# Performance work log

Hardware: AMD Instinct MI355X
Metric: run time of the kernel (lower is better)

## Reference

```python
import jax, jax.numpy as jnp
import numpy as np

B, M, S, P, A, D, H = 16, 8, 100, 40, 3, 128, 8
HD = D // H  # head dim = 16
EPS = 1e-5


def _layernorm(x, g, b):
    mu = jnp.mean(x, axis=-1, keepdims=True)
    var = jnp.mean(jnp.square(x - mu), axis=-1, keepdims=True)
    return (x - mu) * jax.lax.rsqrt(var + EPS) * g + b


def setup_inputs() -> dict:
    key = jax.random.key(0)
    ks = jax.random.split(key, 20)
    attrs = jax.random.normal(ks[0], (B, M, S, P, A), dtype=jnp.float32)
    valid = (jax.random.uniform(ks[1], (B, M, S, P)) < 0.85).astype(jnp.float32)
    roads = jnp.concatenate([attrs, valid[..., None]], axis=-1)  # (B,M,S,P,A+1)
    agents_emb = jax.random.normal(ks[2], (4, B, M, D), dtype=jnp.float32)

    def xavier(k, shape):
        fan_in, fan_out = shape[-2], shape[-1]
        std = float(np.sqrt(2.0 / (fan_in + fan_out)))
        return jax.random.normal(k, shape, dtype=jnp.float32) * std

    return {
        "roads": roads,
        "agents_emb": agents_emb,
        "map_seeds": xavier(ks[3], (1, 1, D)),
        "lin_w": xavier(ks[4], (A, D)), "lin_b": jnp.zeros((D,)),
        "wq": xavier(ks[5], (D, D)), "wk": xavier(ks[6], (D, D)), "wv": xavier(ks[7], (D, D)),
        "bq": jnp.zeros((D,)), "bk": jnp.zeros((D,)), "bv": jnp.zeros((D,)),
        "out_w": xavier(ks[8], (D, D)), "out_b": jnp.zeros((D,)),
        "ln1_g": jnp.ones((D,)), "ln1_b": jnp.zeros((D,)),
        "w1": xavier(ks[9], (D, 3 * D)), "b1": jnp.zeros((3 * D,)),
        "w2": xavier(ks[10], (3 * D, D)), "b2": jnp.zeros((D,)),
        "ln2_g": jnp.ones((D,)), "ln2_b": jnp.zeros((D,)),
    }


def reference(roads, agents_emb, map_seeds, lin_w, lin_b, wq, wk, wv, bq, bk, bv,
              out_w, out_b, ln1_g, ln1_b, w1, b1, w2, b2, ln2_g, ln2_b):
    N = B * M * S
    last = roads[..., -1]  # (B,M,S,P), exact 0/1 existence flags
    # --- masks (True = padded / ignore) ---
    seg_mask = jnp.sum(last, axis=3) == 0  # (B,M,S)
    pts_mask = (1.0 - last).astype(bool).reshape(N, P)
    all_pts = jnp.all(pts_mask, axis=-1)
    pts_mask = pts_mask.at[:, 0].set(pts_mask[:, 0] & ~all_pts)  # unmask pt 0 of empty segs
    all_seg = jnp.all(seg_mask, axis=-1)
    seg_mask = seg_mask.at[:, :, 0].set(seg_mask[:, :, 0] & ~all_seg)

    # --- point feature projection ---
    feats = roads[..., :A].reshape(N, P, A) @ lin_w + lin_b  # (N,P,D)

    # --- single-query multi-head attention pooling (eval mode: no dropout) ---
    q = (map_seeds.reshape(D) @ wq + bq).reshape(H, HD)  # shared seed query
    k = (feats @ wk + bk).reshape(N, P, H, HD)
    v = (feats @ wv + bv).reshape(N, P, H, HD)
    scores = jnp.einsum('hd,nphd->nhp', q, k) * (HD ** -0.5)  # (N,H,P)
    scores = jnp.where(pts_mask[:, None, :], -1e9, scores)
    attn = jax.nn.softmax(scores, axis=-1)
    ctx = jnp.einsum('nhp,nphd->nhd', attn, v).reshape(N, D)
    emb = _layernorm(ctx @ out_w + out_b, ln1_g, ln1_b)  # (N,D)

    # --- FFN + residual + norm (eval mode: no dropout) ---
    ffn = jax.nn.relu(emb @ w1 + b1) @ w2 + b2
    emb2 = _layernorm(emb + ffn, ln2_g, ln2_b)

    out = emb2.reshape(B, M, S, D).transpose(2, 0, 1, 3)  # (S,B,M,D)
    return out, seg_mask
```

## Files before the change

kernel.cpp:

```cpp
#include <hip/hip_runtime.h>

namespace {
constexpr int Sn = 100;
constexpr int Nn = 12800;
constexpr int OUT0 = 1638400;
}

using bf16x8 = __attribute__((ext_vector_type(8))) short;
using f32x4  = __attribute__((ext_vector_type(4))) float;
#define MFMA16(a, b, c) __builtin_amdgcn_mfma_f32_16x16x32_bf16((a), (b), (c), 0, 0, 0)

__device__ __forceinline__ unsigned short f2bf(float x) {
  unsigned int u = __float_as_uint(x);
  return (unsigned short)((u + 0x7FFFu + ((u >> 16) & 1u)) >> 16);
}
__device__ __forceinline__ float bf2f(unsigned short h) {
  return __uint_as_float(((unsigned int)h) << 16);
}

__global__ __launch_bounds__(128) void k0_precompute(
    const float* __restrict__ ms, const float* __restrict__ wq,
    const float* __restrict__ wk, const float* __restrict__ bq,
    const float* __restrict__ bk, const float* __restrict__ lin_w,
    const float* __restrict__ lin_b, const float* __restrict__ wv,
    const float* __restrict__ bv, const float* __restrict__ out_w,
    float* __restrict__ W4qk, unsigned short* __restrict__ Tf) {
  const int t = threadIdx.x;
  if (blockIdx.x < 8) {
    const int h = blockIdx.x;
    __shared__ float q[128];
    __shared__ float qkh[128];
    __shared__ float qbkh;
    __shared__ float part[128];
    float s = bq[t];
    for (int c = 0; c < 128; ++c) s += ms[c] * wq[c * 128 + t];
    q[t] = s;
    __syncthreads();
    float a = 0.f;
#pragma unroll
    for (int j = 0; j < 16; ++j) a += q[h * 16 + j] * wk[t * 128 + h * 16 + j];
    qkh[t] = a * 0.25f;
    if (t == 0) {
      float b = 0.f;
#pragma unroll
      for (int j = 0; j < 16; ++j) b += q[h * 16 + j] * bk[h * 16 + j];
      qbkh = b * 0.25f;
    }
    __syncthreads();
    const int j = t >> 5, cp = t & 31;
    float p = 0.f;
    for (int c = cp * 4; c < cp * 4 + 4; ++c) {
      const float w4 = (j < 3) ? lin_w[j * 128 + c] : lin_b[c];
      p += w4 * qkh[c];
    }
    part[t] = p;
    __syncthreads();
    if (t < 4) {
      float sum = 0.f;
      for (int i = 0; i < 32; ++i) sum += part[t * 32 + i];
      if (t == 3) sum += qbkh;
      W4qk[t * 8 + h] = sum;
    }
  } else {
    const int hj = blockIdx.x - 8;
    const int h = hj >> 2, j = hj & 3;
    __shared__ float part[128];
    __shared__ float w4wv[16];
    const int cp = t & 7;
    float p = 0.f;
    for (int c = cp * 16; c < cp * 16 + 16; ++c) {
      const float w4 = (j < 3) ? lin_w[j * 128 + c] : lin_b[c];
      p += w4 * wv[c * 128 + (h * 16 + (t >> 3))];
    }
    part[t] = p;
    __syncthreads();
    if (t < 16) {
      float sum = 0.f;
      for (int i = 0; i < 8; ++i) sum += part[t * 8 + i];
      if (j == 3) sum += bv[h * 16 + t];
      w4wv[t] = sum;
    }
    __syncthreads();
    float acc = 0.f;
#pragma unroll
    for (int e2 = 0; e2 < 16; ++e2) acc += w4wv[e2] * out_w[(h * 16 + e2) * 128 + t];
    const int ntT = t >> 4, n16T = t & 15;
    const int quadT = hj >> 3, jT = hj & 7;
    const int slot = ntT * 1024 + (quadT * 16 + n16T) * 8 + jT;
    const unsigned short hh = f2bf(acc);
    Tf[slot] = hh;
    Tf[slot + 512] = f2bf(acc - bf2f(hh));
  }
}

__global__ __launch_bounds__(256) void k0b_repack(
    const float* __restrict__ w1, const float* __restrict__ w2,
    unsigned short* __restrict__ w1f, unsigned short* __restrict__ w2f) {
  const int gid = blockIdx.x * 256 + threadIdx.x;
  const int tile = gid >> 6, lane = gid & 63;
  const int quad = lane >> 4, n16 = lane & 15;
  unsigned short hi[8], lo[8];
  unsigned short* dst;
  if (tile < 96) {
    const int nt = tile >> 2, kk = tile & 3;
    const int n = nt * 16 + n16;
#pragma unroll
    for (int j = 0; j < 8; ++j) {
      const int k = kk * 32 + quad * 8 + j;
      const float v = w1[k * 384 + n];
      hi[j] = f2bf(v); lo[j] = f2bf(v - bf2f(hi[j]));
    }
    dst = w1f + (size_t)tile * 1024 + lane * 8;
  } else {
    const int t2 = tile - 96;
    const int nt2 = t2 / 12, kk2 = t2 % 12;
    const int n = nt2 * 16 + n16;
#pragma unroll
    for (int j = 0; j < 8; ++j) {
      const int k = kk2 * 32 + quad * 8 + j;
      const float v = w2[k * 128 + n];
      hi[j] = f2bf(v); lo[j] = f2bf(v - bf2f(hi[j]));
    }
    dst = w2f + (size_t)(tile - 96) * 1024 + lane * 8;
  }
#pragma unroll
  for (int j = 0; j < 8; ++j) { dst[j] = hi[j]; dst[512 + j] = lo[j]; }
}

__global__ __launch_bounds__(256, 4) void k_all(
    const float* __restrict__ roads, const float* __restrict__ W4qk_g,
    const unsigned short* __restrict__ Tf, const float* __restrict__ out_b,
    const float* __restrict__ ln1_g, const float* __restrict__ ln1_b,
    const unsigned short* __restrict__ w1f, const unsigned short* __restrict__ w2f,
    const float* __restrict__ b1, const float* __restrict__ b2,
    const float* __restrict__ ln2_g, const float* __restrict__ ln2_b,
    float* __restrict__ out) {
  const int t = threadIdx.x;
  const int n0 = blockIdx.x * 16;

  __shared__ union {
    float4 pts[640];
    __align__(16) unsigned short A2[12288];
  } u;
  __shared__ __align__(16) unsigned short A1[4096];
  __shared__ __align__(16) unsigned short ApF[1024];
  __shared__ float w4qk_l[32];
  __shared__ float lnr[16][4][2];

  for (int i = t; i < 640; i += 256)
    u.pts[i] = ((const float4*)roads)[(size_t)n0 * 40 + i];
  if (t < 32) w4qk_l[t] = W4qk_g[t];
  __syncthreads();

  {
    const int sh = t >> 1, seg = sh >> 3, h = sh & 7;
    const int p0 = (t & 1) * 20;
    const float wa = w4qk_l[h], wb = w4qk_l[8 + h];
    const float wc = w4qk_l[16 + h], wd = w4qk_l[24 + h];
    float ax = 0.f, ay = 0.f, az = 0.f, den = 0.f;
    int nv = 0;
    for (int p = p0; p < p0 + 20; ++p) {
      const float4 pt = u.pts[seg * 40 + p];
      if (pt.w != 0.f) {
        const float e = __expf(wd + pt.x * wa + pt.y * wb + pt.z * wc);
        ax += e * pt.x; ay += e * pt.y; az += e * pt.z; den += e; ++nv;
      }
    }
    ax += __shfl_xor(ax, 1); ay += __shfl_xor(ay, 1); az += __shfl_xor(az, 1);
    den += __shfl_xor(den, 1); nv += __shfl_xor(nv, 1);
    if ((t & 1) == 0) {
      if (nv == 0) {
        const float4 z = u.pts[seg * 40];
        ax = z.x; ay = z.y; az = z.z; den = 1.f;
      }
      const float inv = 1.f / den;
      const float v[4] = {ax * inv, ay * inv, az * inv, 1.f};
      ushort4 hi, lo;
      unsigned short* hp = (unsigned short*)&hi;
      unsigned short* lp = (unsigned short*)&lo;
#pragma unroll
      for (int c = 0; c < 4; ++c) { hp[c] = f2bf(v[c]); lp[c] = f2bf(v[c] - bf2f(hp[c])); }
      const int slot = ((h >> 1) * 16 + seg) * 8 + (h & 1) * 4;
      *(ushort4*)&ApF[slot] = hi;
      *(ushort4*)&ApF[512 + slot] = lo;
      if (h == 0) out[OUT0 + n0 + seg] = (nv == 0) ? 1.f : 0.f;
    }
  }
  __syncthreads();

  const int w = t >> 6, lane = t & 63;
  const int quad = lane >> 4, nlane = lane & 15;

  float embv[2][4];
  {
    const bf16x8 ahi = *(const bf16x8*)&ApF[lane * 8];
    const bf16x8 alo = *(const bf16x8*)&ApF[512 + lane * 8];
#pragma unroll
    for (int n2 = 0; n2 < 2; ++n2) {
      const int nt = w * 2 + n2;
      const unsigned short* tp = Tf + (size_t)nt * 1024;
      const bf16x8 bhi = *(const bf16x8*)(tp + lane * 8);
      const bf16x8 blo = *(const bf16x8*)(tp + 512 + lane * 8);
      f32x4 acc = (f32x4){0.f, 0.f, 0.f, 0.f};
      acc = MFMA16(alo, bhi, acc);
      acc = MFMA16(ahi, blo, acc);
      acc = MFMA16(ahi, bhi, acc);
      const float ob = out_b[nt * 16 + nlane];
#pragma unroll
      for (int r = 0; r < 4; ++r) embv[n2][r] = acc[r] + ob;
    }
#pragma unroll
    for (int r = 0; r < 4; ++r) {
      float s = embv[0][r] + embv[1][r];
      float v = embv[0][r] * embv[0][r] + embv[1][r] * embv[1][r];
#pragma unroll
      for (int m = 1; m < 16; m <<= 1) { s += __shfl_xor(s, m); v += __shfl_xor(v, m); }
      if (nlane == 0) { lnr[quad * 4 + r][w][0] = s; lnr[quad * 4 + r][w][1] = v; }
    }
  }
  __syncthreads();
#pragma unroll
  for (int r = 0; r < 4; ++r) {
    const int row = quad * 4 + r;
    const float mu = (lnr[row][0][0] + lnr[row][1][0] + lnr[row][2][0] + lnr[row][3][0]) * (1.f / 128.f);
    const float msq = (lnr[row][0][1] + lnr[row][1][1] + lnr[row][2][1] + lnr[row][3][1]) * (1.f / 128.f);
    const float rstd = rsqrtf(msq - mu * mu + 1e-5f);
#pragma unroll
    for (int n2 = 0; n2 < 2; ++n2) {
      const int col = (w * 2 + n2) * 16 + nlane;
      const float e = (embv[n2][r] - mu) * rstd * ln1_g[col] + ln1_b[col];
      const unsigned short hh = f2bf(e), hl = f2bf(e - bf2f(hh));
      const int kk = col >> 5, q2 = (col >> 3) & 3, j = col & 7;
      const int idx = kk * 512 + (q2 * 16 + row) * 8 + j;
      A1[idx] = hh; A1[2048 + idx] = hl;
    }
  }
  __syncthreads();

#pragma unroll
  for (int nti = 0; nti < 6; ++nti) {
    const int nt = w * 6 + nti;
    f32x4 acc = (f32x4){0.f, 0.f, 0.f, 0.f};
#pragma unroll
    for (int kk = 0; kk < 4; ++kk) {
      const bf16x8 ahi = *(const bf16x8*)&A1[kk * 512 + lane * 8];
      const bf16x8 alo = *(const bf16x8*)&A1[2048 + kk * 512 + lane * 8];
      const unsigned short* wp = w1f + (size_t)(nt * 4 + kk) * 1024;
      const bf16x8 bhi = *(const bf16x8*)(wp + lane * 8);
      const bf16x8 blo = *(const bf16x8*)(wp + 512 + lane * 8);
      acc = MFMA16(alo, bhi, acc);
      acc = MFMA16(ahi, blo, acc);
      acc = MFMA16(ahi, bhi, acc);
    }
    const int col = nt * 16 + nlane;
    const float bias = b1[col];
    const int kk2 = col >> 5, qA = (col >> 3) & 3, jA = col & 7;
#pragma unroll
    for (int r = 0; r < 4; ++r) {
      const float h = fmaxf(acc[r] + bias, 0.f);
      const unsigned short hh = f2bf(h), hl = f2bf(h - bf2f(hh));
      const int idx = kk2 * 512 + (qA * 16 + quad * 4 + r) * 8 + jA;
      u.A2[idx] = hh; u.A2[6144 + idx] = hl;
    }
  }
  __syncthreads();

  f32x4 acc2[2];
  acc2[0] = (f32x4){0.f, 0.f, 0.f, 0.f};
  acc2[1] = (f32x4){0.f, 0.f, 0.f, 0.f};
#pragma unroll 4
  for (int kk2 = 0; kk2 < 12; ++kk2) {
    const bf16x8 ahi = *(const bf16x8*)&u.A2[kk2 * 512 + lane * 8];
    const bf16x8 alo = *(const bf16x8*)&u.A2[6144 + kk2 * 512 + lane * 8];
#pragma unroll
    for (int n2 = 0; n2 < 2; ++n2) {
      const unsigned short* wp = w2f + (size_t)((w * 2 + n2) * 12 + kk2) * 1024;
      const bf16x8 bhi = *(const bf16x8*)(wp + lane * 8);
      const bf16x8 blo = *(const bf16x8*)(wp + 512 + lane * 8);
      acc2[n2] = MFMA16(alo, bhi, acc2[n2]);
      acc2[n2] = MFMA16(ahi, blo, acc2[n2]);
      acc2[n2] = MFMA16(ahi, bhi, acc2[n2]);
    }
  }

  float y[2][4];
#pragma unroll
  for (int n2 = 0; n2 < 2; ++n2) {
    const int col = (w * 2 + n2) * 16 + nlane;
    const float bb = b2[col];
    const int kk = col >> 5, q2 = (col >> 3) & 3, j = col & 7;
#pragma unroll
    for (int r = 0; r < 4; ++r) {
      const int idx = kk * 512 + (q2 * 16 + quad * 4 + r) * 8 + j;
      y[n2][r] = acc2[n2][r] + bb + bf2f(A1[idx]) + bf2f(A1[2048 + idx]);
    }
  }
#pragma unroll
  for (int r = 0; r < 4; ++r) {
    float s = y[0][r] + y[1][r];
    float v = y[0][r] * y[0][r] + y[1][r] * y[1][r];
#pragma unroll
    for (int m = 1; m < 16; m <<= 1) { s += __shfl_xor(s, m); v += __shfl_xor(v, m); }
    if (nlane == 0) { lnr[quad * 4 + r][w][0] = s; lnr[quad * 4 + r][w][1] = v; }
  }
  __syncthreads();
#pragma unroll
  for (int r = 0; r < 4; ++r) {
    const int row = quad * 4 + r;
    const float mu = (lnr[row][0][0] + lnr[row][1][0] + lnr[row][2][0] + lnr[row][3][0]) * (1.f / 128.f);
    const float msq = (lnr[row][0][1] + lnr[row][1][1] + lnr[row][2][1] + lnr[row][3][1]) * (1.f / 128.f);
    const float rstd = rsqrtf(msq - mu * mu + 1e-5f);
    const int n = n0 + row, si = n % 100, bm = n / 100;
#pragma unroll
    for (int n2 = 0; n2 < 2; ++n2) {
      const int col = (w * 2 + n2) * 16 + nlane;
      out[(size_t)si * 16384 + bm * 128 + col] =
          (y[n2][r] - mu) * rstd * ln2_g[col] + ln2_b[col];
    }
  }
}

__global__ void k2_fix_segmask(float* __restrict__ out) {
  const int bm = blockIdx.x, t = threadIdx.x;
  const float* base = out + OUT0 + bm * Sn;
  const float a = base[t];
  const float b = (t < 36) ? base[64 + t] : 0.f;
  const unsigned long long m = __ballot((a != 0.f) || (b != 0.f));
  if (t == 0 && m == 0ULL) out[OUT0 + bm * Sn] = 0.f;
}

extern "C" void kernel_launch(void* const* d_in, const int* in_sizes, int n_in,
                              void* d_out, int out_size, void* d_ws, size_t ws_size,
                              hipStream_t stream) {
  const float* roads = (const float*)d_in[0];
  const float* ms    = (const float*)d_in[2];
  const float* lin_w = (const float*)d_in[3];
  const float* lin_b = (const float*)d_in[4];
  const float* wq    = (const float*)d_in[5];
  const float* wk    = (const float*)d_in[6];
  const float* wv    = (const float*)d_in[7];
  const float* bq    = (const float*)d_in[8];
  const float* bk    = (const float*)d_in[9];
  const float* bv    = (const float*)d_in[10];
  const float* out_w = (const float*)d_in[11];
  const float* out_b = (const float*)d_in[12];
  const float* ln1_g = (const float*)d_in[13];
  const float* ln1_b = (const float*)d_in[14];
  const float* w1    = (const float*)d_in[15];
  const float* b1    = (const float*)d_in[16];
  const float* w2    = (const float*)d_in[17];
  const float* b2    = (const float*)d_in[18];
  const float* ln2_g = (const float*)d_in[19];
  const float* ln2_b = (const float*)d_in[20];

  float* out  = (float*)d_out;
  float* W4qk = (float*)d_ws;
  unsigned short* w1f = (unsigned short*)(W4qk + 32);
  unsigned short* w2f = w1f + 96 * 1024;
  unsigned short* Tf  = w2f + 96 * 1024;

  k0_precompute<<<40, 128, 0, stream>>>(ms, wq, wk, bq, bk, lin_w, lin_b, wv, bv, out_w, W4qk, Tf);
  k0b_repack<<<48, 256, 0, stream>>>(w1, w2, w1f, w2f);
  k_all<<<Nn / 16, 256, 0, stream>>>(roads, W4qk, Tf, out_b, ln1_g, ln1_b,
                                     w1f, w2f, b1, b2, ln2_g, ln2_b, out);
  k2_fix_segmask<<<128, 64, 0, stream>>>(out);
}
```

Baseline: 127.0 us.

## Fuse precompute, repack, main and segmask kernels into one launch with flag sync

Merges the weight-precompute, weight-repack, main compute and segment-mask fixup kernels into a single launch. The first 88 blocks act as producers and publish release flags; consumer blocks spin on those flags with acquire loads before using the derived weights. The separate segmask kernel is replaced by per-(b,m) atomic counters that the consumer blocks update at the end. The aim is to remove three kernel launches and their serialization gaps. In exchange it adds spin-wait and deadlock risk if consumers are resident before producers run. Flags are never reset between calls, and the counter reset can race with consumer atomics.

```diff
diff --git a/kernel.cpp b/kernel.cpp
--- a/kernel.cpp
+++ b/kernel.cpp
@@ -4,6 +4,8 @@
 constexpr int Sn = 100;
 constexpr int Nn = 12800;
 constexpr int OUT0 = 1638400;
+constexpr int NPROD = 88;
+constexpr unsigned MAGIC = 0x9E3779B9u;
 }
 
 using bf16x8 = __attribute__((ext_vector_type(8))) short;
@@ -18,138 +20,154 @@
   return __uint_as_float(((unsigned int)h) << 16);
 }
 
-__global__ __launch_bounds__(128) void k0_precompute(
+__global__ __launch_bounds__(256, 4) void k_fused(
+    const float* __restrict__ roads,
     const float* __restrict__ ms, const float* __restrict__ wq,
     const float* __restrict__ wk, const float* __restrict__ bq,
     const float* __restrict__ bk, const float* __restrict__ lin_w,
     const float* __restrict__ lin_b, const float* __restrict__ wv,
     const float* __restrict__ bv, const float* __restrict__ out_w,
-    float* __restrict__ W4qk, unsigned short* __restrict__ Tf) {
-  const int t = threadIdx.x;
-  if (blockIdx.x < 8) {
-    const int h = blockIdx.x;
-    __shared__ float q[128];
-    __shared__ float qkh[128];
-    __shared__ float qbkh;
-    __shared__ float part[128];
-    float s = bq[t];
-    for (int c = 0; c < 128; ++c) s += ms[c] * wq[c * 128 + t];
-    q[t] = s;
-    __syncthreads();
-    float a = 0.f;
-#pragma unroll
-    for (int j = 0; j < 16; ++j) a += q[h * 16 + j] * wk[t * 128 + h * 16 + j];
-    qkh[t] = a * 0.25f;
-    if (t == 0) {
-      float b = 0.f;
-#pragma unroll
-      for (int j = 0; j < 16; ++j) b += q[h * 16 + j] * bk[h * 16 + j];
-      qbkh = b * 0.25f;
-    }
-    __syncthreads();
-    const int j = t >> 5, cp = t & 31;
-    float p = 0.f;
-    for (int c = cp * 4; c < cp * 4 + 4; ++c) {
-      const float w4 = (j < 3) ? lin_w[j * 128 + c] : lin_b[c];
-      p += w4 * qkh[c];
-    }
-    part[t] = p;
-    __syncthreads();
-    if (t < 4) {
-      float sum = 0.f;
-      for (int i = 0; i < 32; ++i) sum += part[t * 32 + i];
-      if (t == 3) sum += qbkh;
-      W4qk[t * 8 + h] = sum;
-    }
-  } else {
-    const int hj = blockIdx.x - 8;
-    const int h = hj >> 2, j = hj & 3;
-    __shared__ float part[128];
-    __shared__ float w4wv[16];
-    const int cp = t & 7;
-    float p = 0.f;
-    for (int c = cp * 16; c < cp * 16 + 16; ++c) {
-      const float w4 = (j < 3) ? lin_w[j * 128 + c] : lin_b[c];
-      p += w4 * wv[c * 128 + (h * 16 + (t >> 3))];
-    }
-    part[t] = p;
-    __syncthreads();
-    if (t < 16) {
-      float sum = 0.f;
-      for (int i = 0; i < 8; ++i) sum += part[t * 8 + i];
-      if (j == 3) sum += bv[h * 16 + t];
-      w4wv[t] = sum;
-    }
-    __syncthreads();
-    float acc = 0.f;
-#pragma unroll
-    for (int e2 = 0; e2 < 16; ++e2) acc += w4wv[e2] * out_w[(h * 16 + e2) * 128 + t];
-    const int ntT = t >> 4, n16T = t & 15;
-    const int quadT = hj >> 3, jT = hj & 7;
-    const int slot = ntT * 1024 + (quadT * 16 + n16T) * 8 + jT;
-    const unsigned short hh = f2bf(acc);
-    Tf[slot] = hh;
-    Tf[slot + 512] = f2bf(acc - bf2f(hh));
-  }
-}
-
-__global__ __launch_bounds__(256) void k0b_repack(
-    const float* __restrict__ w1, const float* __restrict__ w2,
-    unsigned short* __restrict__ w1f, unsigned short* __restrict__ w2f) {
-  const int gid = blockIdx.x * 256 + threadIdx.x;
-  const int tile = gid >> 6, lane = gid & 63;
-  const int quad = lane >> 4, n16 = lane & 15;
-  unsigned short hi[8], lo[8];
-  unsigned short* dst;
-  if (tile < 96) {
-    const int nt = tile >> 2, kk = tile & 3;
-    const int n = nt * 16 + n16;
-#pragma unroll
-    for (int j = 0; j < 8; ++j) {
-      const int k = kk * 32 + quad * 8 + j;
-      const float v = w1[k * 384 + n];
-      hi[j] = f2bf(v); lo[j] = f2bf(v - bf2f(hi[j]));
-    }
-    dst = w1f + (size_t)tile * 1024 + lane * 8;
-  } else {
-    const int t2 = tile - 96;
-    const int nt2 = t2 / 12, kk2 = t2 % 12;
-    const int n = nt2 * 16 + n16;
-#pragma unroll
-    for (int j = 0; j < 8; ++j) {
-      const int k = kk2 * 32 + quad * 8 + j;
-      const float v = w2[k * 128 + n];
-      hi[j] = f2bf(v); lo[j] = f2bf(v - bf2f(hi[j]));
-    }
-    dst = w2f + (size_t)(tile - 96) * 1024 + lane * 8;
-  }
-#pragma unroll
-  for (int j = 0; j < 8; ++j) { dst[j] = hi[j]; dst[512 + j] = lo[j]; }
-}
-
-__global__ __launch_bounds__(256, 4) void k_all(
-    const float* __restrict__ roads, const float* __restrict__ W4qk_g,
-    const unsigned short* __restrict__ Tf, const float* __restrict__ out_b,
+    const float* __restrict__ out_b,
     const float* __restrict__ ln1_g, const float* __restrict__ ln1_b,
-    const unsigned short* __restrict__ w1f, const unsigned short* __restrict__ w2f,
-    const float* __restrict__ b1, const float* __restrict__ b2,
+    const float* __restrict__ w1g, const float* __restrict__ b1,
+    const float* __restrict__ w2g, const float* __restrict__ b2,
     const float* __restrict__ ln2_g, const float* __restrict__ ln2_b,
+    unsigned* __restrict__ flags, unsigned* __restrict__ bmcnt,
+    float* __restrict__ W4qk, unsigned short* __restrict__ w1f,
+    unsigned short* __restrict__ w2f, unsigned short* __restrict__ Tf,
     float* __restrict__ out) {
   const int t = threadIdx.x;
-  const int n0 = blockIdx.x * 16;
+  const int bid = blockIdx.x;
 
   __shared__ union {
     float4 pts[640];
     __align__(16) unsigned short A2[12288];
+    struct { float q[128]; float qkh[128]; float part[128]; float qbkh; } pq;
+    struct { float part[128]; float w4wv[16]; } pt;
   } u;
   __shared__ __align__(16) unsigned short A1[4096];
   __shared__ __align__(16) unsigned short ApF[1024];
   __shared__ float w4qk_l[32];
   __shared__ float lnr[16][4][2];
+  __shared__ unsigned char empt_s[16];
+
+  if (bid < NPROD) {
+    if (bid < 8) {
+      const int h = bid;
+      if (t < 128) {
+        float s = bq[t];
+        for (int c = 0; c < 128; ++c) s += ms[c] * wq[c * 128 + t];
+        u.pq.q[t] = s;
+      }
+      __syncthreads();
+      if (t < 128) {
+        float a = 0.f;
+#pragma unroll
+        for (int j = 0; j < 16; ++j) a += u.pq.q[h * 16 + j] * wk[t * 128 + h * 16 + j];
+        u.pq.qkh[t] = a * 0.25f;
+        if (t == 0) {
+          float b = 0.f;
+#pragma unroll
+          for (int j = 0; j < 16; ++j) b += u.pq.q[h * 16 + j] * bk[h * 16 + j];
+          u.pq.qbkh = b * 0.25f;
+        }
+      }
+      __syncthreads();
+      if (t < 128) {
+        const int j = t >> 5, cp = t & 31;
+        float p = 0.f;
+        for (int c = cp * 4; c < cp * 4 + 4; ++c) {
+          const float w4 = (j < 3) ? lin_w[j * 128 + c] : lin_b[c];
+          p += w4 * u.pq.qkh[c];
+        }
+        u.pq.part[t] = p;
+      }
+      __syncthreads();
+      if (t < 4) {
+        float sum = 0.f;
+        for (int i = 0; i < 32; ++i) sum += u.pq.part[t * 32 + i];
+        if (t == 3) sum += u.pq.qbkh;
+        W4qk[t * 8 + h] = sum;
+      }
+      if (bid == 0 && t < 128) bmcnt[t] = 0u;
+    } else if (bid < 40) {
+      const int hj = bid - 8;
+      const int h = hj >> 2, j = hj & 3;
+      if (t < 128) {
+        const int cp = t & 7;
+        float p = 0.f;
+        for (int c = cp * 16; c < cp * 16 + 16; ++c) {
+          const float w4 = (j < 3) ? lin_w[j * 128 + c] : lin_b[c];
+          p += w4 * wv[c * 128 + (h * 16 + (t >> 3))];
+        }
+        u.pt.part[t] = p;
+      }
+      __syncthreads();
+      if (t < 16) {
+        float sum = 0.f;
+        for (int i = 0; i < 8; ++i) sum += u.pt.part[t * 8 + i];
+        if (j == 3) sum += bv[h * 16 + t];
+        u.pt.w4wv[t] = sum;
+      }
+      __syncthreads();
+      if (t < 128) {
+        float acc = 0.f;
+#pragma unroll
+        for (int e2 = 0; e2 < 16; ++e2) acc += u.pt.w4wv[e2] * out_w[(h * 16 + e2) * 128 + t];
+        const int ntT = t >> 4, n16T = t & 15;
+        const int quadT = hj >> 3;
+        const int slot = ntT * 1024 + (quadT * 16 + n16T) * 8 + (hj & 7);
+        const unsigned short hh = f2bf(acc);
+        Tf[slot] = hh;
+        Tf[slot + 512] = f2bf(acc - bf2f(hh));
+      }
+    } else {
+      const int gid = (bid - 40) * 256 + t;
+      const int tile = gid >> 6, lane = gid & 63;
+      const int quad = lane >> 4, n16 = lane & 15;
+      unsigned short hi[8], lo[8];
+      unsigned short* dst;
+      if (tile < 96) {
+        const int nt = tile >> 2, kk = tile & 3;
+        const int n = nt * 16 + n16;
+#pragma unroll
+        for (int j = 0; j < 8; ++j) {
+          const int k = kk * 32 + quad * 8 + j;
+          const float v = w1g[k * 384 + n];
+          hi[j] = f2bf(v); lo[j] = f2bf(v - bf2f(hi[j]));
+        }
+        dst = w1f + (size_t)tile * 1024 + lane * 8;
+      } else {
+        const int t2 = tile - 96;
+        const int nt2 = t2 / 12, kk2 = t2 % 12;
+        const int n = nt2 * 16 + n16;
+#pragma unroll
+        for (int j = 0; j < 8; ++j) {
+          const int k = kk2 * 32 + quad * 8 + j;
+          const float v = w2g[k * 128 + n];
+          hi[j] = f2bf(v); lo[j] = f2bf(v - bf2f(hi[j]));
+        }
+        dst = w2f + (size_t)(tile - 96) * 1024 + lane * 8;
+      }
+#pragma unroll
+      for (int j = 0; j < 8; ++j) { dst[j] = hi[j]; dst[512 + j] = lo[j]; }
+    }
+    __threadfence();
+    __syncthreads();
+    if (t == 0)
+      __hip_atomic_store(&flags[bid], MAGIC, __ATOMIC_RELEASE, __HIP_MEMORY_SCOPE_AGENT);
+    return;
+  }
+
+  const int cid = bid - NPROD;
+  const int n0 = cid * 16;
 
   for (int i = t; i < 640; i += 256)
     u.pts[i] = ((const float4*)roads)[(size_t)n0 * 40 + i];
-  if (t < 32) w4qk_l[t] = W4qk_g[t];
+  if (t < 8)
+    while (__hip_atomic_load(&flags[t], __ATOMIC_ACQUIRE, __HIP_MEMORY_SCOPE_AGENT) != MAGIC) {}
+  __syncthreads();
+  if (t < 32) w4qk_l[t] = W4qk[t];
   __syncthreads();
 
   {
@@ -183,9 +201,14 @@
       const int slot = ((h >> 1) * 16 + seg) * 8 + (h & 1) * 4;
       *(ushort4*)&ApF[slot] = hi;
       *(ushort4*)&ApF[512 + slot] = lo;
-      if (h == 0) out[OUT0 + n0 + seg] = (nv == 0) ? 1.f : 0.f;
-    }
-  }
+      if (h == 0) {
+        out[OUT0 + n0 + seg] = (nv == 0) ? 1.f : 0.f;
+        empt_s[seg] = (nv == 0) ? 1 : 0;
+      }
+    }
+  }
+  if (t < 80)
+    while (__hip_atomic_load(&flags[8 + t], __ATOMIC_ACQUIRE, __HIP_MEMORY_SCOPE_AGENT) != MAGIC) {}
   __syncthreads();
 
   const int w = t >> 6, lane = t & 63;
@@ -318,15 +341,23 @@
           (y[n2][r] - mu) * rstd * ln2_g[col] + ln2_b[col];
     }
   }
-}
-
-__global__ void k2_fix_segmask(float* __restrict__ out) {
-  const int bm = blockIdx.x, t = threadIdx.x;
-  const float* base = out + OUT0 + bm * Sn;
-  const float a = base[t];
-  const float b = (t < 36) ? base[64 + t] : 0.f;
-  const unsigned long long m = __ballot((a != 0.f) || (b != 0.f));
-  if (t == 0 && m == 0ULL) out[OUT0 + bm * Sn] = 0.f;
+
+  if (t == 0) {
+    __threadfence();
+    int i = 0;
+    while (i < 16) {
+      const int bm = (n0 + i) / 100;
+      const int lim = (bm + 1) * 100 - n0;
+      const int end = lim < 16 ? lim : 16;
+      unsigned cnt = 0, emp = 0;
+      for (; i < end; ++i) { ++cnt; emp += empt_s[i]; }
+      const unsigned add = cnt + (emp << 8);
+      const unsigned now =
+          __hip_atomic_fetch_add(&bmcnt[bm], add, __ATOMIC_ACQ_REL, __HIP_MEMORY_SCOPE_AGENT) + add;
+      if ((now & 0xFFu) == 100u && (now >> 8) == 100u)
+        __hip_atomic_store(&out[OUT0 + bm * Sn], 0.f, __ATOMIC_RELEASE, __HIP_MEMORY_SCOPE_AGENT);
+    }
+  }
 }
 
 extern "C" void kernel_launch(void* const* d_in, const int* in_sizes, int n_in,
@@ -353,15 +384,16 @@
   const float* ln2_g = (const float*)d_in[19];
   const float* ln2_b = (const float*)d_in[20];
 
-  float* out  = (float*)d_out;
-  float* W4qk = (float*)d_ws;
+  float* out = (float*)d_out;
+  unsigned* flags = (unsigned*)d_ws;
+  unsigned* bmcnt = flags + 128;
+  float* W4qk = (float*)(bmcnt + 128);
   unsigned short* w1f = (unsigned short*)(W4qk + 32);
   unsigned short* w2f = w1f + 96 * 1024;
   unsigned short* Tf  = w2f + 96 * 1024;
 
-  k0_precompute<<<40, 128, 0, stream>>>(ms, wq, wk, bq, bk, lin_w, lin_b, wv, bv, out_w, W4qk, Tf);
-  k0b_repack<<<48, 256, 0, stream>>>(w1, w2, w1f, w2f);
-  k_all<<<Nn / 16, 256, 0, stream>>>(roads, W4qk, Tf, out_b, ln1_g, ln1_b,
-                                     w1f, w2f, b1, b2, ln2_g, ln2_b, out);
-  k2_fix_segmask<<<128, 64, 0, stream>>>(out);
-}
+  k_fused<<<NPROD + Nn / 16, 256, 0, stream>>>(
+      roads, ms, wq, wk, bq, bk, lin_w, lin_b, wv, bv, out_w, out_b,
+      ln1_g, ln1_b, w1, b1, w2, b2, ln2_g, ln2_b,
+      flags, bmcnt, W4qk, w1f, w2f, Tf, out);
+}
```

After: 252.5 us. 98.8% more time.
